# Kernel tuning notes

Measured on AMD Instinct MI355X. Metric: run time of the kernel, lower is better.

The kernel has to match this reference:

```python
import jax, jax.numpy as jnp
import numpy as np
from jax import lax

T, B, M, N, D, DA, H, W = 32, 8, 256, 256, 684, 512, 12, 48
QC_CH = 512  # hard-coded coverage conv channels in the module


def setup_inputs() -> dict:
    key = jax.random.key(0)
    ks = iter(jax.random.split(key, 64))
    f = lambda shape, s=0.05: jax.random.normal(next(ks), shape, dtype=jnp.float32) * s
    inp = {
        'rembedding': f((T, B, M), 1.0),
        're_embedding': f((T, B, M), 1.0),
        'ly_mask': jnp.ones((T, B), jnp.float32),
        'context': f((B, D, H, W), 1.0),
        'context_mask': jnp.ones((B, H, W), jnp.float32),
        'init_state': f((B, N), 1.0),
        # fc_Wyz/Wyr/Wyh : Linear(2m -> n)
        'Wyz_w': f((N, 2 * M)), 'Wyz_b': jnp.zeros((N,), jnp.float32),
        'Wyr_w': f((N, 2 * M)), 'Wyr_b': jnp.zeros((N,), jnp.float32),
        'Wyh_w': f((N, 2 * M)), 'Wyh_b': jnp.zeros((N,), jnp.float32),
        # fc_Uhz0/Uhr0/Uhh0 : Linear(n -> n, bias=False)
        'Uhz0_w': f((N, N)), 'Uhr0_w': f((N, N)), 'Uhh0_w': f((N, N)),
        # conv_UaC : Conv2d(D, da, 1)
        'UaC_w': f((DA, D)), 'UaC_b': jnp.zeros((DA,), jnp.float32),
        # fc_WaC : Linear(n -> da, bias=False)
        'WaC_w': f((DA, N)),
        # conv_QC : Conv2d(1, 512, 3, padding=1, bias=False)
        'QC_w': f((QC_CH, 1, 3, 3)),
        # fc_UfC : Linear(512 -> da)
        'UfC_w': f((DA, QC_CH)), 'UfC_b': jnp.zeros((DA,), jnp.float32),
        # fc_vaC : Linear(da -> 1)
        'vaC_w': f((1, DA)), 'vaC_b': jnp.zeros((1,), jnp.float32),
        # fc_Uhz2/Uhr2/Uhh2 : Linear(n -> n)
        'Uhz2_w': f((N, N)), 'Uhz2_b': jnp.zeros((N,), jnp.float32),
        'Uhr2_w': f((N, N)), 'Uhr2_b': jnp.zeros((N,), jnp.float32),
        'Uhh2_w': f((N, N)), 'Uhh2_b': jnp.zeros((N,), jnp.float32),
        # fc_Wcz/Wcr/Wch : Linear(D -> n, bias=False)
        'Wcz_w': f((N, D)), 'Wcr_w': f((N, D)), 'Wch_w': f((N, D)),
        # parent positions into the ctC buffer (valid parents are <= current step)
        'rp': jax.random.randint(next(ks), (T, B), 0, T, dtype=jnp.int32),
    }
    return inp


def _forward(rembedding, re_embedding, ly_mask, context, context_mask, init_state,
             Wyz_w, Wyz_b, Wyr_w, Wyr_b, Wyh_w, Wyh_b,
             Uhz0_w, Uhr0_w, Uhh0_w,
             UaC_w, UaC_b, WaC_w, QC_w, UfC_w, UfC_b, vaC_w, vaC_b,
             Uhz2_w, Uhz2_b, Uhr2_w, Uhr2_b, Uhh2_w, Uhh2_b,
             Wcz_w, Wcr_w, Wch_w, rp):
    n_steps, n_samples = rembedding.shape[0], rembedding.shape[1]
    Hc, Wc = context.shape[2], context.shape[3]
    n = init_state.shape[1]
    d = context.shape[1]

    # pctx_ = conv_UaC(context).permute(2,3,0,1)  -> [H, W, B, da]
    pctx = jnp.einsum('bdhw,ad->hwba', context, UaC_w) + UaC_b
    cmask = context_mask.transpose(1, 2, 0)  # [H, W, B]

    emb = jnp.concatenate([rembedding, re_embedding], axis=2)  # [T, B, 2m]
    sbz = emb @ Wyz_w.T + Wyz_b
    sbr = emb @ Wyr_w.T + Wyr_b
    sbh = emb @ Wyh_w.T + Wyh_b

    batch_idx = jnp.arange(n_samples)

    def step(carry, xs):
        h_, ap_, buf = carry  # h_: [B,n], ap_: [B,H,W], buf: [T+1,B,D]
        z_i, r_i, hh_i, lm, rpos, i = xs
        # gather parent contexts from the running ctC buffer (before this step)
        ctP = buf[rpos, batch_idx]  # [B, D]
        # first GRU cell
        z0 = jax.nn.sigmoid(h_ @ Uhz0_w.T + z_i)
        r0 = jax.nn.sigmoid(h_ @ Uhr0_w.T + r_i)
        h0p = jnp.tanh((h_ @ Uhh0_w.T) * r0 + hh_i)
        h0 = z0 * h_ + (1.0 - z0) * h0p
        h0 = lm[:, None] * h0 + (1.0 - lm)[:, None] * h_
        # coverage attention
        query = h0 @ WaC_w.T  # [B, da]
        cover = lax.conv_general_dilated(
            ap_[:, None, :, :], QC_w, (1, 1), ((1, 1), (1, 1)),
            dimension_numbers=('NCHW', 'OIHW', 'NCHW'))  # [B,512,H,W]
        ccov = jnp.einsum('bchw,ac->hwba', cover, UfC_w) + UfC_b  # [H,W,B,da]
        score = jnp.tanh(pctx + query[None, None, :, :] + ccov)  # [H,W,B,da]
        alpha = (score @ vaC_w.T + vaC_b)[..., 0]  # [H,W,B]
        alpha = jnp.exp(alpha - jnp.max(alpha))
        alpha = alpha * cmask
        alpha = alpha / jnp.sum(alpha, axis=(0, 1))[None, None, :] + 1e-10
        alpha_bhw = alpha.transpose(2, 0, 1)  # [B,H,W]
        ap = ap_ + alpha_bhw
        ctC = jnp.einsum('bdhw,bhw->bd', context, alpha_bhw)  # [B, D]
        # second GRU cell conditioned on the context vector
        z2 = jax.nn.sigmoid(h0 @ Uhz2_w.T + Uhz2_b + ctC @ Wcz_w.T)
        r2 = jax.nn.sigmoid(h0 @ Uhr2_w.T + Uhr2_b + ctC @ Wcr_w.T)
        h2p = jnp.tanh((h0 @ Uhh2_w.T + Uhh2_b) * r2 + ctC @ Wch_w.T)
        h2 = z2 * h0 + (1.0 - z2) * h2p
        h2 = lm[:, None] * h2 + (1.0 - lm)[:, None] * h0
        buf = lax.dynamic_update_slice_in_dim(buf, ctC[None], i + 1, axis=0)
        return (h2, ap, buf), (h2, ctC, ctP, alpha_bhw, ap)

    ap0 = jnp.zeros((n_samples, Hc, Wc), rembedding.dtype)
    buf0 = jnp.zeros((n_steps + 1, n_samples, d), rembedding.dtype)
    xs = (sbz, sbr, sbh, ly_mask, rp, jnp.arange(n_steps))
    _, (h2ts, ctCs, ctPs, calphas, calpha_pasts) = lax.scan(
        step, (init_state, ap0, buf0), xs)
    return h2ts, ctCs, ctPs, calphas, calpha_pasts


def reference(rembedding, re_embedding, ly_mask, context, context_mask, init_state,
              Wyz_w, Wyz_b, Wyr_w, Wyr_b, Wyh_w, Wyh_b,
              Uhz0_w, Uhr0_w, Uhh0_w,
              UaC_w, UaC_b, WaC_w, QC_w, UfC_w, UfC_b, vaC_w, vaC_b,
              Uhz2_w, Uhz2_b, Uhr2_w, Uhr2_b, Uhh2_w, Uhh2_b,
              Wcz_w, Wcr_w, Wch_w, rp):
    return _forward(rembedding, re_embedding, ly_mask, context, context_mask, init_state,
                    Wyz_w, Wyz_b, Wyr_w, Wyr_b, Wyh_w, Wyh_b,
                    Uhz0_w, Uhr0_w, Uhh0_w,
                    UaC_w, UaC_b, WaC_w, QC_w, UfC_w, UfC_b, vaC_w, vaC_b,
                    Uhz2_w, Uhz2_b, Uhr2_w, Uhr2_b, Uhh2_w, Uhh2_b,
                    Wcz_w, Wcr_w, Wch_w, rp)
```

## Files before the change

### kernel.cpp

```cpp
#include <hip/hip_runtime.h>
#include <stdint.h>

typedef unsigned short u16;
typedef unsigned int   u32;

#define TB_ 8
#define NN_ 256
#define DD_ 684
#define PP_ 576

#define OFF_SB    0u
#define OFF_TRAN  0u
#define OFF_BUF   786432u
#define OFF_PCTX  1486848u
#define OFF_FKT   10924032u
#define OFF_RAWP  10942464u
#define OFF_H     11237376u
#define OFF_H0    11245568u
#define OFF_EAL   11253760u
#define OFF_CTR   11272192u
#define OFF_FLG   11274240u
#define WS_NEED   11274256u

#define OFF_H2   0
#define OFF_CTC  65536
#define OFF_CTP  240640
#define OFF_AL   415744
#define OFF_APO  563200

__device__ __forceinline__ float b2f(u16 v){ union{u32 i; float f;} x; x.i = ((u32)v)<<16; return x.f; }
__device__ __forceinline__ float gld(const void* p, size_t i, int f32){
  if (f32) return ((const float*)p)[i];
  return b2f(((const u16*)p)[i]);
}
__device__ __forceinline__ float bl(u32 v){ union{u32 i; float f;} x; x.i = v<<16; return x.f; }
__device__ __forceinline__ float bh(u32 v){ union{u32 i; float f;} x; x.i = v & 0xFFFF0000u; return x.f; }

__device__ __forceinline__ float aload(const float* p){
  u32 v = __hip_atomic_load((const u32*)p, __ATOMIC_RELAXED, __HIP_MEMORY_SCOPE_AGENT);
  union{u32 i; float f;} x; x.i = v; return x.f;
}
__device__ __forceinline__ void astore(float* p, float v){
  union{float f; u32 i;} x; x.f = v;
  __hip_atomic_store((u32*)p, x.i, __ATOMIC_RELAXED, __HIP_MEMORY_SCOPE_AGENT);
}

__device__ __forceinline__ float rcpf(float x){ return __builtin_amdgcn_rcpf(x); }
__device__ __forceinline__ float sigm(float x){
  x = fminf(fmaxf(x, -30.f), 30.f);
  return rcpf(1.f + __expf(-x));
}
__device__ __forceinline__ float tanh_c(float x){
  x = fminf(fmaxf(x, -15.f), 15.f);
  float e = __expf(2.f*x);
  return 1.f - 2.f*rcpf(e + 1.f);
}

__device__ __forceinline__ float dot8(uint4 u, const float* s){
  float a = fmaf(bl(u.x), s[0], bh(u.x)*s[1]);
  a = fmaf(bl(u.y), s[2], a); a = fmaf(bh(u.y), s[3], a);
  a = fmaf(bl(u.z), s[4], a); a = fmaf(bh(u.z), s[5], a);
  a = fmaf(bl(u.w), s[6], a); a = fmaf(bh(u.w), s[7], a);
  return a;
}
__device__ __forceinline__ float dot4t(uint2 u, const float* s, float a){
  a = fmaf(bl(u.x), s[0], a); a = fmaf(bh(u.x), s[1], a);
  a = fmaf(bl(u.y), s[2], a); a = fmaf(bh(u.y), s[3], a);
  return a;
}
__device__ __forceinline__ float dotf(const float* w, const float* s, int n){
  float a = 0.f;
  #pragma unroll 4
  for (int k=0;k<n;k+=4){
    float4 u = *(const float4*)(w+k);
    a = fmaf(u.x, s[k], a);   a = fmaf(u.y, s[k+1], a);
    a = fmaf(u.z, s[k+2], a); a = fmaf(u.w, s[k+3], a);
  }
  return a;
}
__device__ __forceinline__ float dotw(const void* W, size_t row_off, const float* s, int n, int f32){
  if (f32) return dotf((const float*)W + row_off, s, n);
  const u16* r = (const u16*)W + row_off;
  float a = 0.f;
  int k = 0;
  for (; k+8 <= n; k += 8) a += dot8(*(const uint4*)(r+k), s+k);
  if (k < n) a = dot4t(*(const uint2*)(r+k), s+k, a);
  return a;
}

__global__ void k_detect(const u16* __restrict__ ctx_u16, int* __restrict__ flag){
  __shared__ int cnt;
  if (threadIdx.x == 0) cnt = 0;
  __syncthreads();
  int bad = 0;
  for (int k = threadIdx.x; k < 512; k += 256){
    u16 v = ctx_u16[k];
    int e = (v >> 7) & 0xFF;
    bool sane = (v == 0u) || (v == 0x8000u) || (e >= 102 && e <= 141);
    if (!sane) bad++;
  }
  atomicAdd(&cnt, bad);
  __syncthreads();
  if (threadIdx.x == 0) flag[0] = (cnt > 64) ? 1 : 0;
}


__global__ __launch_bounds__(256) void k_init(float* __restrict__ buf, float* __restrict__ eal,
                                              u32* __restrict__ ctr, float* __restrict__ h,
                                              const void* __restrict__ init_state,
                                              const int* __restrict__ flag){
  const int f32 = flag[0];
  int i = blockIdx.x*blockDim.x + threadIdx.x;
  int stride = gridDim.x*blockDim.x;
  for (int k=i; k<32*TB_*DD_; k+=stride) buf[k] = 0.f;
  for (int k=i; k<TB_*PP_;    k+=stride) eal[k] = 0.f;
  for (int k=i; k<TB_*64;     k+=stride) ctr[k] = 0u;
  for (int k=i; k<TB_*NN_;    k+=stride) h[k]   = gld(init_state, k, f32);
}

__global__ __launch_bounds__(256) void k_tran(const void* __restrict__ UaC_w,
                                              float* __restrict__ UaCT,
                                              const int* __restrict__ flag){
  const int f32 = flag[0];
  size_t i = (size_t)blockIdx.x*256 + threadIdx.x;
  if (i >= (size_t)512*DD_) return;
  int a = (int)(i / DD_), d = (int)(i - (size_t)a*DD_);
  UaCT[(size_t)d*512 + a] = gld(UaC_w, i, f32);
}

__global__ __launch_bounds__(256) void k_fk(const void* __restrict__ QC, const void* __restrict__ UfC,
                                            float* __restrict__ FKt, const int* __restrict__ flag){
  const int f32 = flag[0];
  __shared__ float qc[4608];
  int tid = threadIdx.x;
  for (int k=tid;k<4608;k+=256) qc[k] = gld(QC, k, f32);
  __syncthreads();
  const int lane = tid & 63;
  const int wid = blockIdx.x*4 + (tid>>6);
  for (int rr=0; rr<4; rr++){
    const int a = wid*4 + rr;
    float acc[9];
    #pragma unroll
    for (int tt=0;tt<9;tt++) acc[tt]=0.f;
    #pragma unroll
    for (int k=0;k<8;k++){
      int c = lane + k*64;
      float v = gld(UfC, (size_t)a*512 + c, f32);
      const float* q = &qc[c*9];
      #pragma unroll
      for (int tt=0;tt<9;tt++) acc[tt] = fmaf(v, q[tt], acc[tt]);
    }
    #pragma unroll
    for (int off=1; off<64; off<<=1){
      #pragma unroll
      for (int tt=0;tt<9;tt++) acc[tt] += __shfl_xor(acc[tt], off, 64);
    }
    #pragma unroll
    for (int tt=0;tt<9;tt++) if (lane == tt) FKt[tt*512 + a] = acc[tt];
  }
}

__global__ __launch_bounds__(512) void k_pctx2(const void* __restrict__ context,
    const float* __restrict__ UaCT, const void* __restrict__ UaC_b, const void* __restrict__ UfC_b,
    float* __restrict__ pctx, const int* __restrict__ flag){
  const int f32 = flag[0];
  const int blk = blockIdx.x;
  const int b = blk / 18;
  const int pbase = (blk - b*18) * 32;
  __shared__ float ctx[32][DD_];
  const int tid = threadIdx.x;
  for (int k=tid; k<32*DD_; k+=512){
    int p = k & 31, d = k >> 5;
    ctx[p][d] = gld(context, ((size_t)(b*DD_+d))*PP_ + pbase + p, f32);
  }
  __syncthreads();
  const int a = tid;
  float acc[32];
  #pragma unroll
  for (int p=0;p<32;p++) acc[p] = 0.f;
  for (int d=0; d<DD_; d+=4){
    float w0 = UaCT[(size_t)(d+0)*512 + a];
    float w1 = UaCT[(size_t)(d+1)*512 + a];
    float w2 = UaCT[(size_t)(d+2)*512 + a];
    float w3 = UaCT[(size_t)(d+3)*512 + a];
    #pragma unroll
    for (int p=0;p<32;p++){
      float4 c = *(const float4*)(&ctx[p][d]);
      float t = acc[p];
      t = fmaf(c.x, w0, t); t = fmaf(c.y, w1, t);
      t = fmaf(c.z, w2, t); t = fmaf(c.w, w3, t);
      acc[p] = t;
    }
  }
  float bias = gld(UaC_b, a, f32) + gld(UfC_b, a, f32);
  #pragma unroll
  for (int p=0;p<32;p++)
    pctx[((size_t)(b*PP_ + pbase + p))*512 + a] = acc[p] + bias;
}

__global__ __launch_bounds__(256) void k_sb(const void* __restrict__ remb, const void* __restrict__ re_emb,
    const void* __restrict__ Wz, const void* __restrict__ bz,
    const void* __restrict__ Wr, const void* __restrict__ br,
    const void* __restrict__ Wh, const void* __restrict__ bhh,
    float* __restrict__ sb, const int* __restrict__ flag){
  const int f32 = flag[0];
  int blk = blockIdx.x;
  int g = blk >> 8;
  int tb = blk & 255; int t = tb >> 3; int b = tb & 7;
  __shared__ float emb[512];
  int tid = threadIdx.x;
  emb[tid]     = gld(remb,   (size_t)(t*8+b)*256 + tid, f32);
  emb[tid+256] = gld(re_emb, (size_t)(t*8+b)*256 + tid, f32);
  __syncthreads();
  const void* W = (g==0?Wz:(g==1?Wr:Wh));
  const void* bias = (g==0?bz:(g==1?br:bhh));
  float acc = gld(bias, tid, f32) + dotw(W, (size_t)tid*512, emb, 512, f32);
  sb[(((size_t)g*32+t)*8+b)*256 + tid] = acc;
}


__device__ __forceinline__ void group_bar(u32* ctr, u32 target){
  __syncthreads();
  if (threadIdx.x == 0){
    __hip_atomic_fetch_add(ctr, 1u, __ATOMIC_RELAXED, __HIP_MEMORY_SCOPE_AGENT);
    while (__hip_atomic_load(ctr, __ATOMIC_RELAXED, __HIP_MEMORY_SCOPE_AGENT) < target)
      __builtin_amdgcn_s_sleep(2);
  }
  __syncthreads();
}

__global__ __launch_bounds__(256, 1) void k_main(
    const void* __restrict__ ly_mask, const void* __restrict__ context, const void* __restrict__ cmask,
    const void* __restrict__ Uhz0, const void* __restrict__ Uhr0, const void* __restrict__ Uhh0,
    const void* __restrict__ WaC, const void* __restrict__ vaC_w, const void* __restrict__ vaC_b,
    const void* __restrict__ Uhz2, const void* __restrict__ Uhz2_b,
    const void* __restrict__ Uhr2, const void* __restrict__ Uhr2_b,
    const void* __restrict__ Uhh2, const void* __restrict__ Uhh2_b,
    const void* __restrict__ Wcz, const void* __restrict__ Wcr, const void* __restrict__ Wch,
    const int* __restrict__ rp,
    const float* __restrict__ pctx, const float* __restrict__ sb, const float* __restrict__ FKt,
    float* buf, float* h_ws, float* h0_ws, float* ealpha, float* rawp, u32* ctrs,
    float* out, const int* __restrict__ flag)
{
  const int f32 = flag[0];
  const int tid = threadIdx.x;
  const int b = blockIdx.x >> 4;
  const int j = blockIdx.x & 15;
  const int abase = j*32, nbase = j*16;

  __shared__ float hprev[NN_], h0_lds[NN_];
  __shared__ float ap_lds[PP_], al_lds[PP_], cm_lds[PP_];
  __shared__ float ctc_lds[DD_];
  __shared__ float fk_lds[9*32], vac_lds[32], q_lds[32], qpart[256];
  __shared__ float g1[48], u2l[48], wcl[48];
  __shared__ float red16[16];

  for (int k=tid; k<288; k+=256) fk_lds[k] = FKt[(k>>5)*512 + abase + (k&31)];
  if (tid < 32) vac_lds[tid] = gld(vaC_w, abase + tid, f32);
  cm_lds[tid]     = gld(cmask, b*PP_ + tid, f32);
  cm_lds[tid+256] = gld(cmask, b*PP_ + tid + 256, f32);
  if (tid < 64) cm_lds[tid+512] = gld(cmask, b*PP_ + tid + 512, f32);
  ap_lds[tid] = 0.f; ap_lds[tid+256] = 0.f;
  if (tid < 64) ap_lds[tid+512] = 0.f;
  const float vb = gld(vaC_b, 0, f32);

  u32* ctr = ctrs + b*64;
  float* psum_ws = (float*)(ctr + 16);
  u32 bar_t = 0;
  const int p0 = tid, p1 = tid + 256, p2 = tid + 512;
  const bool has3 = (tid < 64);
  const int pown = j*36;

  for (int t=0; t<32; t++){
    const float lm = gld(ly_mask, t*8+b, f32);

    hprev[tid] = aload(&h_ws[b*256 + tid]);
    __syncthreads();

    if (tid < 192){
      int item = tid >> 2, q = tid & 3;
      int g = item >> 4, nl = item & 15;
      int n = nbase + nl;
      const void* U = (g==0 ? Uhz0 : (g==1 ? Uhr0 : Uhh0));
      float acc = dotw(U, (size_t)n*256 + q*64, &hprev[q*64], 64, f32);
      acc += __shfl_xor(acc,1,64); acc += __shfl_xor(acc,2,64);
      if (q==0) g1[g*16+nl] = acc;
    }
    __syncthreads();
    if (tid < 16){
      int n = nbase + tid;
      float hp = hprev[n];
      float z0 = sigm(g1[tid]    + sb[(((size_t)t)*8+b)*256 + n]);
      float r0 = sigm(g1[16+tid] + sb[(((size_t)(32+t))*8+b)*256 + n]);
      float hc = tanh_c(g1[32+tid]*r0 + sb[(((size_t)(64+t))*8+b)*256 + n]);
      float h0v = z0*hp + (1.f - z0)*hc;
      h0v = lm*h0v + (1.f - lm)*hp;
      astore(&h0_ws[b*256 + n], h0v);
    }
    {
      int rpos = rp[t*8+b];
      if ((unsigned)rpos > 31u) rpos = 31;
      int dbase = j*43, dcnt = (j==15) ? 39 : 43;
      if (tid < dcnt){
        int d = dbase + tid;
        out[OFF_CTP + (t*8+b)*DD_ + d] = aload(&buf[((size_t)rpos*8+b)*DD_ + d]);
      }
    }
    bar_t += 16; group_bar(ctr, bar_t);

    h0_lds[tid] = aload(&h0_ws[b*256 + tid]);
    __syncthreads();
    {
      int ai = tid & 31, nb = tid >> 5;
      qpart[nb*32 + ai] = dotw(WaC, (size_t)(abase+ai)*256 + nb*32, &h0_lds[nb*32], 32, f32);
    }
    __syncthreads();
    if (tid < 32){
      float qv = 0.f;
      #pragma unroll
      for (int nb2=0;nb2<8;nb2++) qv += qpart[nb2*32 + tid];
      q_lds[tid] = qv;
    }
    __syncthreads();
    for (int rep=0; rep<3; rep++){
      int p = tid + rep*256;
      if (p >= PP_) break;
      float PQ[32];
      const float* pc = pctx + ((size_t)(b*PP_ + p))*512 + abase;
      #pragma unroll
      for (int q8=0;q8<8;q8++){
        float4 u = *(const float4*)(pc + q8*4);
        PQ[q8*4+0]=u.x; PQ[q8*4+1]=u.y; PQ[q8*4+2]=u.z; PQ[q8*4+3]=u.w;
      }
      int hh_ = p / 48, ww_ = p - hh_*48;
      #pragma unroll
      for (int kh=0;kh<3;kh++){
        int h2_ = hh_ + kh - 1;
        if ((unsigned)h2_ >= 12u) continue;
        #pragma unroll
        for (int kw=0;kw<3;kw++){
          int w2_ = ww_ + kw - 1;
          if ((unsigned)w2_ >= 48u) continue;
          float av = ap_lds[h2_*48 + w2_];
          const float* fkp = &fk_lds[(kh*3+kw)*32];
          #pragma unroll
          for (int ai=0;ai<32;ai++) PQ[ai] = fmaf(av, fkp[ai], PQ[ai]);
        }
      }
      float racc = 0.f;
      #pragma unroll
      for (int ai=0;ai<32;ai++)
        racc = fmaf(vac_lds[ai], tanh_c(PQ[ai] + q_lds[ai]), racc);
      astore(&rawp[((size_t)(b*16+j))*PP_ + p], racc);
    }
    if (tid < 192){
      int item = tid >> 2, q = tid & 3;
      int g = item >> 4, nl = item & 15;
      int n = nbase + nl;
      const void* U = (g==0 ? Uhz2 : (g==1 ? Uhr2 : Uhh2));
      float acc = dotw(U, (size_t)n*256 + q*64, &h0_lds[q*64], 64, f32);
      acc += __shfl_xor(acc,1,64); acc += __shfl_xor(acc,2,64);
      if (q==0) u2l[g*16+nl] = acc;
    }
    bar_t += 16; group_bar(ctr, bar_t);

    {
      float ev = 0.f;
      if (tid < 36){
        int p = pown + tid;
        float raw = vb;
        #pragma unroll
        for (int j2=0;j2<16;j2++) raw += aload(&rawp[((size_t)(b*16+j2))*PP_ + p]);
        raw = fminf(fmaxf(raw, -60.f), 60.f);
        ev = __expf(raw) * cm_lds[p];
        astore(&ealpha[b*PP_ + p], ev);
      }
      if (tid < 64){
        float s = ev;
        #pragma unroll
        for (int off=1; off<64; off<<=1) s += __shfl_xor(s, off, 64);
        if (tid == 0) astore(&psum_ws[j], s);
      }
    }
    bar_t += 16; group_bar(ctr, bar_t);

    {
      float e0 = aload(&ealpha[b*PP_ + p0]);
      float e1 = aload(&ealpha[b*PP_ + p1]);
      float e2 = has3 ? aload(&ealpha[b*PP_ + p2]) : 0.f;
      if (tid < 16) red16[tid] = aload(&psum_ws[tid]);
      __syncthreads();
      float S = 0.f;
      #pragma unroll
      for (int k=0;k<16;k++) S += red16[k];
      S = fmaxf(S, 1e-30f);
      float inv = rcpf(S);
      float a0 = e0*inv + 1e-10f; al_lds[p0] = a0; ap_lds[p0] += a0;
      float a1 = e1*inv + 1e-10f; al_lds[p1] = a1; ap_lds[p1] += a1;
      if (has3){ float a2 = e2*inv + 1e-10f; al_lds[p2] = a2; ap_lds[p2] += a2; }
    }
    __syncthreads();
    if (tid < 36){
      int p = pown + tid;
      out[OFF_AL  + (t*8+b)*PP_ + p] = al_lds[p];
      out[OFF_APO + (t*8+b)*PP_ + p] = ap_lds[p];
    }
    {
      int dbase = j*43, dcnt = (j==15) ? 39 : 43;
      if (tid < dcnt*4){
        int dd = tid >> 2, q = tid & 3, d = dbase + dd;
        float acc;
        if (f32) acc = dotf((const float*)context + ((size_t)(b*DD_+d))*PP_ + q*144, &al_lds[q*144], 144);
        else {
          const u16* crow = (const u16*)context + ((size_t)(b*DD_+d))*PP_ + q*144;
          acc = 0.f;
          #pragma unroll 6
          for (int k=0;k<144;k+=8) acc += dot8(*(const uint4*)(crow+k), &al_lds[q*144+k]);
        }
        acc += __shfl_xor(acc,1,64); acc += __shfl_xor(acc,2,64);
        if (q==0){
          astore(&out[OFF_CTC + (t*8+b)*DD_ + d], acc);
          if (t < 31) astore(&buf[(((size_t)(t+1))*8+b)*DD_ + d], acc);
        }
      }
    }
    bar_t += 16; group_bar(ctr, bar_t);

    for (int k=tid; k<DD_; k+=256) ctc_lds[k] = aload(&out[OFF_CTC + (t*8+b)*DD_ + k]);
    __syncthreads();
    if (tid < 192){
      int item = tid >> 2, q = tid & 3;
      int g = item >> 4, nl = item & 15;
      int n = nbase + nl;
      const void* W = (g==0 ? Wcz : (g==1 ? Wcr : Wch));
      int base = q*176, cnt = (q==3) ? 156 : 176;
      float acc = dotw(W, (size_t)n*DD_ + base, &ctc_lds[base], cnt, f32);
      acc += __shfl_xor(acc,1,64); acc += __shfl_xor(acc,2,64);
      if (q==0) wcl[g*16+nl] = acc;
    }
    __syncthreads();
    if (tid < 16){
      int n = nbase + tid;
      float h0v = h0_lds[n];
      float z2 = sigm(u2l[tid]    + gld(Uhz2_b, n, f32) + wcl[tid]);
      float r2 = sigm(u2l[16+tid] + gld(Uhr2_b, n, f32) + wcl[16+tid]);
      float hc = tanh_c((u2l[32+tid] + gld(Uhh2_b, n, f32))*r2 + wcl[32+tid]);
      float h2v = z2*h0v + (1.f - z2)*hc;
      h2v = lm*h2v + (1.f - lm)*h0v;
      astore(&h_ws[b*256 + n], h2v);
      out[OFF_H2 + (t*8+b)*256 + n] = h2v;
    }
    bar_t += 16; group_bar(ctr, bar_t);
  }
}


extern "C" void kernel_launch(void* const* d_in, const int* in_sizes, int n_in,
                              void* d_out, int out_size, void* d_ws, size_t ws_size,
                              hipStream_t stream){
  (void)in_sizes; (void)n_in; (void)out_size;
  if (ws_size < WS_NEED) return;

  const void* remb       = d_in[0];
  const void* re_emb     = d_in[1];
  const void* ly_mask    = d_in[2];
  const void* context    = d_in[3];
  const void* cmask      = d_in[4];
  const void* init_state = d_in[5];
  const void* Wyz_w = d_in[6];  const void* Wyz_b = d_in[7];
  const void* Wyr_w = d_in[8];  const void* Wyr_b = d_in[9];
  const void* Wyh_w = d_in[10]; const void* Wyh_b = d_in[11];
  const void* Uhz0  = d_in[12];
  const void* Uhr0  = d_in[13];
  const void* Uhh0  = d_in[14];
  const void* UaC_w = d_in[15]; const void* UaC_b = d_in[16];
  const void* WaC_w = d_in[17];
  const void* QC_w  = d_in[18];
  const void* UfC_w = d_in[19]; const void* UfC_b = d_in[20];
  const void* vaC_w = d_in[21]; const void* vaC_b = d_in[22];
  const void* Uhz2  = d_in[23]; const void* Uhz2_b = d_in[24];
  const void* Uhr2  = d_in[25]; const void* Uhr2_b = d_in[26];
  const void* Uhh2  = d_in[27]; const void* Uhh2_b = d_in[28];
  const void* Wcz   = d_in[29];
  const void* Wcr   = d_in[30];
  const void* Wch   = d_in[31];
  const int*  rp    = (const int*)d_in[32];

  char* ws = (char*)d_ws;
  float* sbp   = (float*)(ws + OFF_SB);
  float* UaCT  = (float*)(ws + OFF_TRAN);
  float* buf   = (float*)(ws + OFF_BUF);
  float* pctx  = (float*)(ws + OFF_PCTX);
  float* FKt   = (float*)(ws + OFF_FKT);
  float* rawp  = (float*)(ws + OFF_RAWP);
  float* h_ws  = (float*)(ws + OFF_H);
  float* h0_ws = (float*)(ws + OFF_H0);
  float* eal   = (float*)(ws + OFF_EAL);
  u32*   ctrs  = (u32*)  (ws + OFF_CTR);
  int*   flag  = (int*)  (ws + OFF_FLG);
  float* out   = (float*)d_out;

  k_detect<<<1, 256, 0, stream>>>((const u16*)context, flag);
  k_tran <<<1368, 256, 0, stream>>>(UaC_w, UaCT, flag);
  k_fk   <<<32,  256, 0, stream>>>(QC_w, UfC_w, FKt, flag);
  k_pctx2<<<144, 512, 0, stream>>>(context, UaCT, UaC_b, UfC_b, pctx, flag);
  k_sb   <<<768, 256, 0, stream>>>(remb, re_emb, Wyz_w, Wyz_b, Wyr_w, Wyr_b, Wyh_w, Wyh_b, sbp, flag);
  k_init <<<256, 256, 0, stream>>>(buf, eal, ctrs, h_ws, init_state, flag);
  k_main <<<128, 256, 0, stream>>>(ly_mask, context, cmask,
                                   Uhz0, Uhr0, Uhh0, WaC_w, vaC_w, vaC_b,
                                   Uhz2, Uhz2_b, Uhr2, Uhr2_b, Uhh2, Uhh2_b,
                                   Wcz, Wcr, Wch, rp,
                                   pctx, sbp, FKt,
                                   buf, h_ws, h0_ws, eal, rawp, ctrs, out, flag);
}
```

Baseline: 1.189 ms.

## Replace group counter barriers with per-block flags and merge prologue kernels

The persistent main kernel drops its shared-counter group barriers in favour of per-block epoch flags polled by a wave. One barrier phase is removed because every block now recomputes the softmax normalisation from the raw partials itself, so the exp/psum workspace round-trip goes away. The prologue kernels are merged (transpose with FK, sb with init), the transpose becomes LDS-tiled, and pctx switches to a 4x16 register tile with float4 loads and stores. The risks are subtle memory-ordering races from relaxed flag stores and redundant exp work in every block.

```diff
diff --git a/kernel.cpp b/kernel.cpp
--- a/kernel.cpp
+++ b/kernel.cpp
@@ -17,8 +17,7 @@
 #define OFF_RAWP  10942464u
 #define OFF_H     11237376u
 #define OFF_H0    11245568u
-#define OFF_EAL   11253760u
-#define OFF_CTR   11272192u
+#define OFF_SYNC  11253760u
 #define OFF_FLG   11274240u
 #define WS_NEED   11274256u
 
@@ -27,6 +26,11 @@
 #define OFF_CTP  240640
 #define OFF_AL   415744
 #define OFF_APO  563200
+
+#define EX_H0 0
+#define EX_RW 1
+#define EX_CT 2
+#define EX_H2 3
 
 __device__ __forceinline__ float b2f(u16 v){ union{u32 i; float f;} x; x.i = ((u32)v)<<16; return x.f; }
 __device__ __forceinline__ float gld(const void* p, size_t i, int f32){
@@ -86,6 +90,19 @@
   for (; k+8 <= n; k += 8) a += dot8(*(const uint4*)(r+k), s+k);
   if (k < n) a = dot4t(*(const uint2*)(r+k), s+k, a);
   return a;
+}
+
+__device__ __forceinline__ void flag_set(u32* f, u32 val){
+  __hip_atomic_store(f, val, __ATOMIC_RELAXED, __HIP_MEMORY_SCOPE_AGENT);
+}
+__device__ __forceinline__ void flag_wait(const u32* fbase, u32 tgt){
+  const u32* f = fbase + (threadIdx.x & 15);
+  while (true){
+    u32 v = __hip_atomic_load(f, __ATOMIC_RELAXED, __HIP_MEMORY_SCOPE_AGENT);
+    if (__all((int)(v >= tgt))) break;
+    __builtin_amdgcn_s_sleep(1);
+  }
+  asm volatile("" ::: "memory");
 }
 
 __global__ void k_detect(const u16* __restrict__ ctx_u16, int* __restrict__ flag){
@@ -104,63 +121,62 @@
   if (threadIdx.x == 0) flag[0] = (cnt > 64) ? 1 : 0;
 }
 
-
-__global__ __launch_bounds__(256) void k_init(float* __restrict__ buf, float* __restrict__ eal,
-                                              u32* __restrict__ ctr, float* __restrict__ h,
-                                              const void* __restrict__ init_state,
-                                              const int* __restrict__ flag){
+__global__ __launch_bounds__(256) void k_pre1(
+    const void* __restrict__ UaC_w, float* __restrict__ UaCT,
+    const void* __restrict__ QC, const void* __restrict__ UfC, float* __restrict__ FKt,
+    const int* __restrict__ flag)
+{
   const int f32 = flag[0];
-  int i = blockIdx.x*blockDim.x + threadIdx.x;
-  int stride = gridDim.x*blockDim.x;
-  for (int k=i; k<32*TB_*DD_; k+=stride) buf[k] = 0.f;
-  for (int k=i; k<TB_*PP_;    k+=stride) eal[k] = 0.f;
-  for (int k=i; k<TB_*64;     k+=stride) ctr[k] = 0u;
-  for (int k=i; k<TB_*NN_;    k+=stride) h[k]   = gld(init_state, k, f32);
-}
-
-__global__ __launch_bounds__(256) void k_tran(const void* __restrict__ UaC_w,
-                                              float* __restrict__ UaCT,
-                                              const int* __restrict__ flag){
-  const int f32 = flag[0];
-  size_t i = (size_t)blockIdx.x*256 + threadIdx.x;
-  if (i >= (size_t)512*DD_) return;
-  int a = (int)(i / DD_), d = (int)(i - (size_t)a*DD_);
-  UaCT[(size_t)d*512 + a] = gld(UaC_w, i, f32);
-}
-
-__global__ __launch_bounds__(256) void k_fk(const void* __restrict__ QC, const void* __restrict__ UfC,
-                                            float* __restrict__ FKt, const int* __restrict__ flag){
-  const int f32 = flag[0];
-  __shared__ float qc[4608];
-  int tid = threadIdx.x;
-  for (int k=tid;k<4608;k+=256) qc[k] = gld(QC, k, f32);
-  __syncthreads();
-  const int lane = tid & 63;
-  const int wid = blockIdx.x*4 + (tid>>6);
-  for (int rr=0; rr<4; rr++){
-    const int a = wid*4 + rr;
-    float acc[9];
-    #pragma unroll
-    for (int tt=0;tt<9;tt++) acc[tt]=0.f;
-    #pragma unroll
-    for (int k=0;k<8;k++){
-      int c = lane + k*64;
-      float v = gld(UfC, (size_t)a*512 + c, f32);
-      const float* q = &qc[c*9];
-      #pragma unroll
-      for (int tt=0;tt<9;tt++) acc[tt] = fmaf(v, q[tt], acc[tt]);
-    }
-    #pragma unroll
-    for (int off=1; off<64; off<<=1){
-      #pragma unroll
-      for (int tt=0;tt<9;tt++) acc[tt] += __shfl_xor(acc[tt], off, 64);
-    }
-    #pragma unroll
-    for (int tt=0;tt<9;tt++) if (lane == tt) FKt[tt*512 + a] = acc[tt];
-  }
-}
-
-__global__ __launch_bounds__(512) void k_pctx2(const void* __restrict__ context,
+  const int tid = threadIdx.x;
+  __shared__ float smem[4608];
+  int bid = blockIdx.x;
+
+  if (bid < 88){
+    int ab = bid / 11, db = bid - ab*11;
+    int tc = tid & 63, tr = tid >> 6;
+    int d0 = db*64, a0 = ab*64;
+    for (int rr = tr; rr < 64; rr += 4){
+      int d = d0 + tc;
+      if (d < DD_) smem[rr*65 + tc] = gld(UaC_w, (size_t)(a0+rr)*DD_ + d, f32);
+    }
+    __syncthreads();
+    for (int rr = tr; rr < 64; rr += 4){
+      int d = d0 + rr;
+      if (d < DD_) UaCT[(size_t)d*512 + a0 + tc] = smem[tc*65 + rr];
+    }
+    return;
+  }
+  bid -= 88;
+  {
+    for (int k=tid;k<4608;k+=256) smem[k] = gld(QC, k, f32);
+    __syncthreads();
+    const int lane = tid & 63;
+    const int wid = bid*4 + (tid>>6);
+    for (int rr=0; rr<4; rr++){
+      const int a = wid*4 + rr;
+      float acc[9];
+      #pragma unroll
+      for (int tt=0;tt<9;tt++) acc[tt]=0.f;
+      #pragma unroll
+      for (int k=0;k<8;k++){
+        int c = lane + k*64;
+        float v = gld(UfC, (size_t)a*512 + c, f32);
+        const float* q = &smem[c*9];
+        #pragma unroll
+        for (int tt=0;tt<9;tt++) acc[tt] = fmaf(v, q[tt], acc[tt]);
+      }
+      #pragma unroll
+      for (int off=1; off<64; off<<=1){
+        #pragma unroll
+        for (int tt=0;tt<9;tt++) acc[tt] += __shfl_xor(acc[tt], off, 64);
+      }
+      #pragma unroll
+      for (int tt=0;tt<9;tt++) if (lane == tt) FKt[tt*512 + a] = acc[tt];
+    }
+  }
+}
+
+__global__ __launch_bounds__(256) void k_pctx2(const void* __restrict__ context,
     const float* __restrict__ UaCT, const void* __restrict__ UaC_b, const void* __restrict__ UfC_b,
     float* __restrict__ pctx, const int* __restrict__ flag){
   const int f32 = flag[0];
@@ -169,65 +185,81 @@
   const int pbase = (blk - b*18) * 32;
   __shared__ float ctx[32][DD_];
   const int tid = threadIdx.x;
-  for (int k=tid; k<32*DD_; k+=512){
+  for (int k=tid; k<32*DD_; k+=256){
     int p = k & 31, d = k >> 5;
     ctx[p][d] = gld(context, ((size_t)(b*DD_+d))*PP_ + pbase + p, f32);
   }
   __syncthreads();
-  const int a = tid;
-  float acc[32];
+  const int a0 = (tid & 127) * 4;
+  const int pr = (tid >> 7) * 16;
+  float acc[16][4];
   #pragma unroll
-  for (int p=0;p<32;p++) acc[p] = 0.f;
+  for (int p=0;p<16;p++){ acc[p][0]=0.f; acc[p][1]=0.f; acc[p][2]=0.f; acc[p][3]=0.f; }
   for (int d=0; d<DD_; d+=4){
-    float w0 = UaCT[(size_t)(d+0)*512 + a];
-    float w1 = UaCT[(size_t)(d+1)*512 + a];
-    float w2 = UaCT[(size_t)(d+2)*512 + a];
-    float w3 = UaCT[(size_t)(d+3)*512 + a];
+    float4 w0 = *(const float4*)&UaCT[(size_t)(d+0)*512 + a0];
+    float4 w1 = *(const float4*)&UaCT[(size_t)(d+1)*512 + a0];
+    float4 w2 = *(const float4*)&UaCT[(size_t)(d+2)*512 + a0];
+    float4 w3 = *(const float4*)&UaCT[(size_t)(d+3)*512 + a0];
     #pragma unroll
-    for (int p=0;p<32;p++){
-      float4 c = *(const float4*)(&ctx[p][d]);
-      float t = acc[p];
-      t = fmaf(c.x, w0, t); t = fmaf(c.y, w1, t);
-      t = fmaf(c.z, w2, t); t = fmaf(c.w, w3, t);
-      acc[p] = t;
-    }
-  }
-  float bias = gld(UaC_b, a, f32) + gld(UfC_b, a, f32);
+    for (int p=0;p<16;p++){
+      float4 c = *(const float4*)(&ctx[pr+p][d]);
+      acc[p][0] = fmaf(c.x, w0.x, acc[p][0]); acc[p][1] = fmaf(c.x, w0.y, acc[p][1]);
+      acc[p][2] = fmaf(c.x, w0.z, acc[p][2]); acc[p][3] = fmaf(c.x, w0.w, acc[p][3]);
+      acc[p][0] = fmaf(c.y, w1.x, acc[p][0]); acc[p][1] = fmaf(c.y, w1.y, acc[p][1]);
+      acc[p][2] = fmaf(c.y, w1.z, acc[p][2]); acc[p][3] = fmaf(c.y, w1.w, acc[p][3]);
+      acc[p][0] = fmaf(c.z, w2.x, acc[p][0]); acc[p][1] = fmaf(c.z, w2.y, acc[p][1]);
+      acc[p][2] = fmaf(c.z, w2.z, acc[p][2]); acc[p][3] = fmaf(c.z, w2.w, acc[p][3]);
+      acc[p][0] = fmaf(c.w, w3.x, acc[p][0]); acc[p][1] = fmaf(c.w, w3.y, acc[p][1]);
+      acc[p][2] = fmaf(c.w, w3.z, acc[p][2]); acc[p][3] = fmaf(c.w, w3.w, acc[p][3]);
+    }
+  }
+  float b0 = gld(UaC_b, a0+0, f32) + gld(UfC_b, a0+0, f32);
+  float b1 = gld(UaC_b, a0+1, f32) + gld(UfC_b, a0+1, f32);
+  float b2 = gld(UaC_b, a0+2, f32) + gld(UfC_b, a0+2, f32);
+  float b3 = gld(UaC_b, a0+3, f32) + gld(UfC_b, a0+3, f32);
   #pragma unroll
-  for (int p=0;p<32;p++)
-    pctx[((size_t)(b*PP_ + pbase + p))*512 + a] = acc[p] + bias;
-}
-
-__global__ __launch_bounds__(256) void k_sb(const void* __restrict__ remb, const void* __restrict__ re_emb,
+  for (int p=0;p<16;p++){
+    float4 v; v.x = acc[p][0]+b0; v.y = acc[p][1]+b1; v.z = acc[p][2]+b2; v.w = acc[p][3]+b3;
+    *(float4*)&pctx[((size_t)(b*PP_ + pbase + pr + p))*512 + a0] = v;
+  }
+}
+
+__global__ __launch_bounds__(256) void k_pre2(
+    const void* __restrict__ remb, const void* __restrict__ re_emb,
     const void* __restrict__ Wz, const void* __restrict__ bz,
     const void* __restrict__ Wr, const void* __restrict__ br,
     const void* __restrict__ Wh, const void* __restrict__ bhh,
-    float* __restrict__ sb, const int* __restrict__ flag){
+    float* __restrict__ sb,
+    float* __restrict__ buf, u32* __restrict__ sync, float* __restrict__ h,
+    const void* __restrict__ init_state,
+    const int* __restrict__ flag)
+{
   const int f32 = flag[0];
-  int blk = blockIdx.x;
-  int g = blk >> 8;
-  int tb = blk & 255; int t = tb >> 3; int b = tb & 7;
-  __shared__ float emb[512];
-  int tid = threadIdx.x;
-  emb[tid]     = gld(remb,   (size_t)(t*8+b)*256 + tid, f32);
-  emb[tid+256] = gld(re_emb, (size_t)(t*8+b)*256 + tid, f32);
-  __syncthreads();
-  const void* W = (g==0?Wz:(g==1?Wr:Wh));
-  const void* bias = (g==0?bz:(g==1?br:bhh));
-  float acc = gld(bias, tid, f32) + dotw(W, (size_t)tid*512, emb, 512, f32);
-  sb[(((size_t)g*32+t)*8+b)*256 + tid] = acc;
-}
-
-
-__device__ __forceinline__ void group_bar(u32* ctr, u32 target){
-  __syncthreads();
-  if (threadIdx.x == 0){
-    __hip_atomic_fetch_add(ctr, 1u, __ATOMIC_RELAXED, __HIP_MEMORY_SCOPE_AGENT);
-    while (__hip_atomic_load(ctr, __ATOMIC_RELAXED, __HIP_MEMORY_SCOPE_AGENT) < target)
-      __builtin_amdgcn_s_sleep(2);
-  }
-  __syncthreads();
-}
+  const int tid = threadIdx.x;
+  int bid = blockIdx.x;
+  if (bid < 768){
+    __shared__ float emb[512];
+    int g = bid >> 8;
+    int tb = bid & 255; int t = tb >> 3; int b = tb & 7;
+    emb[tid]     = gld(remb,   (size_t)(t*8+b)*256 + tid, f32);
+    emb[tid+256] = gld(re_emb, (size_t)(t*8+b)*256 + tid, f32);
+    __syncthreads();
+    const void* W = (g==0?Wz:(g==1?Wr:Wh));
+    const void* bias = (g==0?bz:(g==1?br:bhh));
+    float acc = gld(bias, tid, f32) + dotw(W, (size_t)tid*512, emb, 512, f32);
+    sb[(((size_t)g*32+t)*8+b)*256 + tid] = acc;
+    return;
+  }
+  bid -= 768;
+  {
+    int i = bid*256 + tid;
+    int stride = 256*256;
+    for (int k=i; k<32*TB_*DD_; k+=stride) buf[k] = 0.f;
+    for (int k=i; k<TB_*128;    k+=stride) sync[k] = 0u;
+    for (int k=i; k<TB_*NN_;    k+=stride) h[k]   = gld(init_state, k, f32);
+  }
+}
+
 
 __global__ __launch_bounds__(256, 1) void k_main(
     const void* __restrict__ ly_mask, const void* __restrict__ context, const void* __restrict__ cmask,
@@ -239,7 +271,7 @@
     const void* __restrict__ Wcz, const void* __restrict__ Wcr, const void* __restrict__ Wch,
     const int* __restrict__ rp,
     const float* __restrict__ pctx, const float* __restrict__ sb, const float* __restrict__ FKt,
-    float* buf, float* h_ws, float* h0_ws, float* ealpha, float* rawp, u32* ctrs,
+    float* buf, float* h_ws, float* h0_ws, float* rawp, u32* syncg,
     float* out, const int* __restrict__ flag)
 {
   const int f32 = flag[0];
@@ -253,7 +285,7 @@
   __shared__ float ctc_lds[DD_];
   __shared__ float fk_lds[9*32], vac_lds[32], q_lds[32], qpart[256];
   __shared__ float g1[48], u2l[48], wcl[48];
-  __shared__ float red16[16];
+  __shared__ float red[4];
 
   for (int k=tid; k<288; k+=256) fk_lds[k] = FKt[(k>>5)*512 + abase + (k&31)];
   if (tid < 32) vac_lds[tid] = gld(vaC_w, abase + tid, f32);
@@ -264,16 +296,16 @@
   if (tid < 64) ap_lds[tid+512] = 0.f;
   const float vb = gld(vaC_b, 0, f32);
 
-  u32* ctr = ctrs + b*64;
-  float* psum_ws = (float*)(ctr + 16);
-  u32 bar_t = 0;
+  u32* syncb = syncg + b*128;
   const int p0 = tid, p1 = tid + 256, p2 = tid + 512;
   const bool has3 = (tid < 64);
   const int pown = j*36;
 
   for (int t=0; t<32; t++){
     const float lm = gld(ly_mask, t*8+b, f32);
-
+    const u32 tgt = (u32)(t+1);
+
+    if (t) flag_wait(syncb + EX_H2*16, (u32)t);
     hprev[tid] = aload(&h_ws[b*256 + tid]);
     __syncthreads();
 
@@ -306,8 +338,12 @@
         out[OFF_CTP + (t*8+b)*DD_ + d] = aload(&buf[((size_t)rpos*8+b)*DD_ + d]);
       }
     }
-    bar_t += 16; group_bar(ctr, bar_t);
-
+    if (tid < 64){
+      asm volatile("s_waitcnt vmcnt(0)" ::: "memory");
+      if (tid == 0) flag_set(syncb + EX_H0*16 + j, tgt);
+    }
+
+    flag_wait(syncb + EX_H0*16, tgt);
     h0_lds[tid] = aload(&h0_ws[b*256 + tid]);
     __syncthreads();
     {
@@ -362,42 +398,34 @@
       acc += __shfl_xor(acc,1,64); acc += __shfl_xor(acc,2,64);
       if (q==0) u2l[g*16+nl] = acc;
     }
-    bar_t += 16; group_bar(ctr, bar_t);
-
+    __syncthreads();
+    if (tid == 0) flag_set(syncb + EX_RW*16 + j, tgt);
+
+    flag_wait(syncb + EX_RW*16, tgt);
     {
-      float ev = 0.f;
-      if (tid < 36){
-        int p = pown + tid;
+      float psum = 0.f;
+      for (int rep=0; rep<3; rep++){
+        int p = tid + rep*256;
+        if (p >= PP_) break;
         float raw = vb;
         #pragma unroll
         for (int j2=0;j2<16;j2++) raw += aload(&rawp[((size_t)(b*16+j2))*PP_ + p]);
         raw = fminf(fmaxf(raw, -60.f), 60.f);
-        ev = __expf(raw) * cm_lds[p];
-        astore(&ealpha[b*PP_ + p], ev);
-      }
-      if (tid < 64){
-        float s = ev;
-        #pragma unroll
-        for (int off=1; off<64; off<<=1) s += __shfl_xor(s, off, 64);
-        if (tid == 0) astore(&psum_ws[j], s);
-      }
-    }
-    bar_t += 16; group_bar(ctr, bar_t);
-
+        float e = __expf(raw) * cm_lds[p];
+        al_lds[p] = e; psum += e;
+      }
+      #pragma unroll
+      for (int off=1; off<64; off<<=1) psum += __shfl_xor(psum, off, 64);
+      if ((tid & 63)==0) red[tid>>6] = psum;
+    }
+    __syncthreads();
     {
-      float e0 = aload(&ealpha[b*PP_ + p0]);
-      float e1 = aload(&ealpha[b*PP_ + p1]);
-      float e2 = has3 ? aload(&ealpha[b*PP_ + p2]) : 0.f;
-      if (tid < 16) red16[tid] = aload(&psum_ws[tid]);
-      __syncthreads();
-      float S = 0.f;
-      #pragma unroll
-      for (int k=0;k<16;k++) S += red16[k];
+      float S = red[0] + red[1] + red[2] + red[3];
       S = fmaxf(S, 1e-30f);
       float inv = rcpf(S);
-      float a0 = e0*inv + 1e-10f; al_lds[p0] = a0; ap_lds[p0] += a0;
-      float a1 = e1*inv + 1e-10f; al_lds[p1] = a1; ap_lds[p1] += a1;
-      if (has3){ float a2 = e2*inv + 1e-10f; al_lds[p2] = a2; ap_lds[p2] += a2; }
+      float a0 = al_lds[p0]*inv + 1e-10f; al_lds[p0] = a0; ap_lds[p0] += a0;
+      float a1 = al_lds[p1]*inv + 1e-10f; al_lds[p1] = a1; ap_lds[p1] += a1;
+      if (has3){ float a2 = al_lds[p2]*inv + 1e-10f; al_lds[p2] = a2; ap_lds[p2] += a2; }
     }
     __syncthreads();
     if (tid < 36){
@@ -424,8 +452,10 @@
         }
       }
     }
-    bar_t += 16; group_bar(ctr, bar_t);
-
+    __syncthreads();
+    if (tid == 0) flag_set(syncb + EX_CT*16 + j, tgt);
+
+    flag_wait(syncb + EX_CT*16, tgt);
     for (int k=tid; k<DD_; k+=256) ctc_lds[k] = aload(&out[OFF_CTC + (t*8+b)*DD_ + k]);
     __syncthreads();
     if (tid < 192){
@@ -450,7 +480,10 @@
       astore(&h_ws[b*256 + n], h2v);
       out[OFF_H2 + (t*8+b)*256 + n] = h2v;
     }
-    bar_t += 16; group_bar(ctr, bar_t);
+    if (tid < 64){
+      asm volatile("s_waitcnt vmcnt(0)" ::: "memory");
+      if (tid == 0) flag_set(syncb + EX_H2*16 + j, tgt);
+    }
   }
 }
 
@@ -495,21 +528,19 @@
   float* rawp  = (float*)(ws + OFF_RAWP);
   float* h_ws  = (float*)(ws + OFF_H);
   float* h0_ws = (float*)(ws + OFF_H0);
-  float* eal   = (float*)(ws + OFF_EAL);
-  u32*   ctrs  = (u32*)  (ws + OFF_CTR);
+  u32*   syncg = (u32*)  (ws + OFF_SYNC);
   int*   flag  = (int*)  (ws + OFF_FLG);
   float* out   = (float*)d_out;
 
   k_detect<<<1, 256, 0, stream>>>((const u16*)context, flag);
-  k_tran <<<1368, 256, 0, stream>>>(UaC_w, UaCT, flag);
-  k_fk   <<<32,  256, 0, stream>>>(QC_w, UfC_w, FKt, flag);
-  k_pctx2<<<144, 512, 0, stream>>>(context, UaCT, UaC_b, UfC_b, pctx, flag);
-  k_sb   <<<768, 256, 0, stream>>>(remb, re_emb, Wyz_w, Wyz_b, Wyr_w, Wyr_b, Wyh_w, Wyh_b, sbp, flag);
-  k_init <<<256, 256, 0, stream>>>(buf, eal, ctrs, h_ws, init_state, flag);
+  k_pre1 <<<120, 256, 0, stream>>>(UaC_w, UaCT, QC_w, UfC_w, FKt, flag);
+  k_pctx2<<<144, 256, 0, stream>>>(context, UaCT, UaC_b, UfC_b, pctx, flag);
+  k_pre2 <<<1024, 256, 0, stream>>>(remb, re_emb, Wyz_w, Wyz_b, Wyr_w, Wyr_b, Wyh_w, Wyh_b, sbp,
+                                    buf, syncg, h_ws, init_state, flag);
   k_main <<<128, 256, 0, stream>>>(ly_mask, context, cmask,
                                    Uhz0, Uhr0, Uhh0, WaC_w, vaC_w, vaC_b,
                                    Uhz2, Uhz2_b, Uhr2, Uhr2_b, Uhh2, Uhh2_b,
                                    Wcz, Wcr, Wch, rp,
                                    pctx, sbp, FKt,
-                                   buf, h_ws, h0_ws, eal, rawp, ctrs, out, flag);
-}
+                                   buf, h_ws, h0_ws, rawp, syncg, out, flag);
+}
```

New measurement: 1.241 ms. +4.3%, slower.
